# Performance work log

Hardware: AMD Instinct MI355X
Metric: run time of the kernel (lower is better)

Reference implementation:

```python
import jax, jax.numpy as jnp
import numpy as np

WINDOW_SIZE = 11  # 2*h_patch_size + 1 with h_patch_size=5
SIGMA = 1.5
C1 = 0.01 ** 2
C2 = 0.03 ** 2


def _window2d():
    x = np.arange(WINDOW_SIZE) - WINDOW_SIZE // 2
    g = np.exp(-(x ** 2) / (2.0 * SIGMA ** 2))
    g = g / g.sum()
    w = np.outer(g, g)  # [ws, ws], sums to 1
    return jnp.asarray(w, dtype=jnp.float32)


def setup_inputs() -> dict:
    key = jax.random.key(0)
    k1, k2 = jax.random.split(key)
    n_view, N, n_p, npatch, C = 4, 2048, 16, 121, 3
    img_pred = jax.random.uniform(k1, (n_view, N, n_p, npatch, C), dtype=jnp.float32)
    img_gt = jax.random.uniform(k2, (N, n_p, npatch, C), dtype=jnp.float32)
    return {"img_pred": img_pred, "img_gt": img_gt}


def reference(img_pred, img_gt):
    # img_pred: [n_view, N, n_p, npatch, C]; img_gt: [N, n_p, npatch, C]
    n_view, N, n_p, npatch, C = img_pred.shape
    ps = WINDOW_SIZE  # patch_size == window_size since conv has padding=0 and output is 1x1
    w = _window2d()  # [ps, ps]

    pred = img_pred.reshape(n_view, N, n_p, ps, ps, C)
    gt = img_gt.reshape(1, N, n_p, ps, ps, C)

    # Depthwise 11x11 conv on an 11x11 patch with padding=0 == gaussian-weighted sum.
    def wsum(x):
        return jnp.einsum('vnphwc,hw->vnpc', x, w)

    mu1 = wsum(pred)                      # [n_view, N, n_p, C]
    mu2 = wsum(gt)                        # [1, N, n_p, C]
    mu1_sq = mu1 * mu1
    mu2_sq = mu2 * mu2
    mu1_mu2 = mu1 * mu2
    sigma1_sq = wsum(pred * pred) - mu1_sq
    sigma2_sq = wsum(gt * gt) - mu2_sq    # [1, N, n_p, C]
    sigma12 = wsum(pred * gt) - mu1_mu2   # pred*gt broadcasts over n_view

    ssim_map = ((2.0 * mu1_mu2 + C1) * (2.0 * sigma12 + C2)) / (
        (mu1_sq + mu2_sq + C1) * (sigma1_sq + sigma2_sq + C2))
    return ssim_map.mean(-1)  # [n_view, N, n_p]
```

## Files before the change

### kernel.cpp

```cpp
#include <hip/hip_runtime.h>


static constexpr int N_OUT   = 4 * 2048 * 16;
static constexpr int NP_MASK = 2048 * 16 - 1;

__device__ __constant__ float G11[11] = {
    0.00102838f, 0.00759875f, 0.03600077f, 0.10936070f, 0.21300555f,
    0.26601173f,
    0.21300555f, 0.10936070f, 0.03600077f, 0.00759875f, 0.00102838f
};

__global__ __launch_bounds__(256) void ssim_kernel(
    const float* __restrict__ pred, const float* __restrict__ gt,
    float* __restrict__ out)
{
    const int o = blockIdx.x * 256 + threadIdx.x;
    const float* p = pred + (size_t)o * 363;
    const float* g = gt   + (size_t)(o & NP_MASK) * 363;

    float mu1[3] = {0.f, 0.f, 0.f};
    float mu2[3] = {0.f, 0.f, 0.f};
    float s1 [3] = {0.f, 0.f, 0.f};
    float s2 [3] = {0.f, 0.f, 0.f};
    float s12[3] = {0.f, 0.f, 0.f};

    #pragma unroll 1
    for (int r = 0; r < 11; ++r) {
        const float wr = G11[r];
        const float* pr = p + r * 33;
        const float* gr = g + r * 33;
        #pragma unroll
        for (int col = 0; col < 11; ++col) {
            const float w = wr * G11[col];
            #pragma unroll
            for (int c = 0; c < 3; ++c) {
                const float pv = pr[col * 3 + c];
                const float gv = gr[col * 3 + c];
                mu1[c] += w * pv;
                mu2[c] += w * gv;
                s1 [c] += w * pv * pv;
                s2 [c] += w * gv * gv;
                s12[c] += w * pv * gv;
            }
        }
    }

    const float C1 = 1e-4f;
    const float C2 = 9e-4f;
    float acc = 0.f;
    #pragma unroll
    for (int c = 0; c < 3; ++c) {
        const float m1 = mu1[c], m2 = mu2[c];
        const float m1sq = m1 * m1, m2sq = m2 * m2, m12 = m1 * m2;
        const float sig1  = s1[c]  - m1sq;
        const float sig2  = s2[c]  - m2sq;
        const float sg12  = s12[c] - m12;
        const float num = (2.f * m12 + C1) * (2.f * sg12 + C2);
        const float den = (m1sq + m2sq + C1) * (sig1 + sig2 + C2);
        acc += num / den;
    }
    out[o] = acc * (1.f / 3.f);
}

extern "C" void kernel_launch(void* const* d_in, const int* in_sizes, int n_in,
                              void* d_out, int out_size, void* d_ws, size_t ws_size,
                              hipStream_t stream) {
    const float* pred = (const float*)d_in[0];
    const float* gt   = (const float*)d_in[1];
    float* out        = (float*)d_out;
    ssim_kernel<<<N_OUT / 256, 256, 0, stream>>>(pred, gt, out);
}
```

Measured before the change: 340.2 us.

## Split each patch across 16 lanes with shuffle reduction for coalesced loads

Instead of one thread walking a whole 363-float patch with strided loads, 16 lanes share each patch, each loading a few pixels, and the partial sums are combined with xor shuffles. The 2D Gaussian weights are precomputed into shared memory. The goal is to coalesce global reads, which were badly strided across threads before. The cost is 15 shuffle rounds per patch, 7 of 128 slots padded with zero weights, and most lanes sitting idle during the final SSIM step.

```diff
diff --git a/kernel.cpp b/kernel.cpp
--- a/kernel.cpp
+++ b/kernel.cpp
@@ -10,11 +10,34 @@
     0.21300555f, 0.10936070f, 0.03600077f, 0.00759875f, 0.00102838f
 };
 
+__device__ __forceinline__ float red16(float v) {
+    v += __shfl_xor(v, 1);
+    v += __shfl_xor(v, 2);
+    v += __shfl_xor(v, 4);
+    v += __shfl_xor(v, 8);
+    return v;
+}
+
 __global__ __launch_bounds__(256) void ssim_kernel(
     const float* __restrict__ pred, const float* __restrict__ gt,
     float* __restrict__ out)
 {
-    const int o = blockIdx.x * 256 + threadIdx.x;
+    __shared__ float W[128];
+    const int t = threadIdx.x;
+    if (t < 128) {
+        float w = 0.f;
+        if (t < 121) {
+            const int r = t / 11;
+            const int c = t - r * 11;
+            w = G11[r] * G11[c];
+        }
+        W[t] = w;
+    }
+    __syncthreads();
+
+    const int lane  = t & 15;
+    const int group = t >> 4;
+    const int o     = blockIdx.x * 16 + group;
     const float* p = pred + (size_t)o * 363;
     const float* g = gt   + (size_t)(o & NP_MASK) * 363;
 
@@ -24,42 +47,51 @@
     float s2 [3] = {0.f, 0.f, 0.f};
     float s12[3] = {0.f, 0.f, 0.f};
 
-    #pragma unroll 1
-    for (int r = 0; r < 11; ++r) {
-        const float wr = G11[r];
-        const float* pr = p + r * 33;
-        const float* gr = g + r * 33;
+    #pragma unroll
+    for (int rnd = 0; rnd < 8; ++rnd) {
+        const int pix = lane + rnd * 16;
+        const float w = W[pix];
+        const int pc  = (pix < 121 ? pix : 120) * 3;
+        const float pv[3] = {p[pc], p[pc + 1], p[pc + 2]};
+        const float gv[3] = {g[pc], g[pc + 1], g[pc + 2]};
         #pragma unroll
-        for (int col = 0; col < 11; ++col) {
-            const float w = wr * G11[col];
-            #pragma unroll
-            for (int c = 0; c < 3; ++c) {
-                const float pv = pr[col * 3 + c];
-                const float gv = gr[col * 3 + c];
-                mu1[c] += w * pv;
-                mu2[c] += w * gv;
-                s1 [c] += w * pv * pv;
-                s2 [c] += w * gv * gv;
-                s12[c] += w * pv * gv;
-            }
+        for (int c = 0; c < 3; ++c) {
+            const float tp = w * pv[c];
+            const float tg = w * gv[c];
+            mu1[c] += tp;
+            mu2[c] += tg;
+            s1 [c] = fmaf(tp, pv[c], s1 [c]);
+            s2 [c] = fmaf(tg, gv[c], s2 [c]);
+            s12[c] = fmaf(tp, gv[c], s12[c]);
         }
     }
 
-    const float C1 = 1e-4f;
-    const float C2 = 9e-4f;
-    float acc = 0.f;
     #pragma unroll
     for (int c = 0; c < 3; ++c) {
-        const float m1 = mu1[c], m2 = mu2[c];
-        const float m1sq = m1 * m1, m2sq = m2 * m2, m12 = m1 * m2;
-        const float sig1  = s1[c]  - m1sq;
-        const float sig2  = s2[c]  - m2sq;
-        const float sg12  = s12[c] - m12;
-        const float num = (2.f * m12 + C1) * (2.f * sg12 + C2);
-        const float den = (m1sq + m2sq + C1) * (sig1 + sig2 + C2);
-        acc += num / den;
+        mu1[c] = red16(mu1[c]);
+        mu2[c] = red16(mu2[c]);
+        s1 [c] = red16(s1 [c]);
+        s2 [c] = red16(s2 [c]);
+        s12[c] = red16(s12[c]);
     }
-    out[o] = acc * (1.f / 3.f);
+
+    if (lane == 0) {
+        const float C1 = 1e-4f;
+        const float C2 = 9e-4f;
+        float acc = 0.f;
+        #pragma unroll
+        for (int c = 0; c < 3; ++c) {
+            const float m1 = mu1[c], m2 = mu2[c];
+            const float m1sq = m1 * m1, m2sq = m2 * m2, m12 = m1 * m2;
+            const float sig1 = s1[c]  - m1sq;
+            const float sig2 = s2[c]  - m2sq;
+            const float sg12 = s12[c] - m12;
+            const float num = (2.f * m12 + C1) * (2.f * sg12 + C2);
+            const float den = (m1sq + m2sq + C1) * (sig1 + sig2 + C2);
+            acc += num / den;
+        }
+        out[o] = acc * (1.f / 3.f);
+    }
 }
 
 extern "C" void kernel_launch(void* const* d_in, const int* in_sizes, int n_in,
@@ -68,5 +100,5 @@
     const float* pred = (const float*)d_in[0];
     const float* gt   = (const float*)d_in[1];
     float* out        = (float*)d_out;
-    ssim_kernel<<<N_OUT / 256, 256, 0, stream>>>(pred, gt, out);
+    ssim_kernel<<<N_OUT / 16, 256, 0, stream>>>(pred, gt, out);
 }
```

Result: faster. 293.8 us (-13.6%).

## Cooperate 16 lanes per output with coalesced LDS staging and LDS reduction

Applied to the files above, without the earlier changes.

Replaces the one-thread-per-output scheme, where each thread strided through 1452 bytes and loads were uncoalesced, with 16 lanes per output. Each wave stages four contiguous prediction patches into LDS using coalesced float4 loads. Each lane accumulates pairs of pixels with precomputed weights, and the partial sums are reduced through LDS scratch. It relies on manual lgkmcnt waits rather than barriers, which are valid only because each wave touches its own LDS region. It also adds reduction overhead and sets a launch-bounds occupancy hint.

```diff
diff --git a/kernel.cpp b/kernel.cpp
--- a/kernel.cpp
+++ b/kernel.cpp
@@ -3,6 +3,9 @@
 
 static constexpr int N_OUT   = 4 * 2048 * 16;
 static constexpr int NP_MASK = 2048 * 16 - 1;
+static constexpr int OPB     = 16;
+static constexpr int V4_WAVE = 363;
+static constexpr int LDS_F4  = 4 * V4_WAVE + 2;
 
 __device__ __constant__ float G11[11] = {
     0.00102838f, 0.00759875f, 0.03600077f, 0.10936070f, 0.21300555f,
@@ -10,56 +13,131 @@
     0.21300555f, 0.10936070f, 0.03600077f, 0.00759875f, 0.00102838f
 };
 
-__global__ __launch_bounds__(256) void ssim_kernel(
+__global__ __launch_bounds__(256, 6) void ssim_kernel(
     const float* __restrict__ pred, const float* __restrict__ gt,
     float* __restrict__ out)
 {
-    const int o = blockIdx.x * 256 + threadIdx.x;
-    const float* p = pred + (size_t)o * 363;
-    const float* g = gt   + (size_t)(o & NP_MASK) * 363;
+    __shared__ float4 predS4[LDS_F4];
 
+    const int t      = threadIdx.x;
+    const int wave   = t >> 6;
+    const int lane64 = t & 63;
+    const int lane   = t & 15;
+    const int group  = t >> 4;
+    const int o      = blockIdx.x * OPB + group;
+
+    const float* g = gt + (size_t)(o & NP_MASK) * 363;
+    float gv[4][6];
+    #pragma unroll
+    for (int r = 0; r < 4; ++r) {
+        const int k  = lane + r * 16;
+        const int kc = (k < 60 ? k : 60);
+        const float* gk = g + 6 * kc;
+        gv[r][0] = gk[0]; gv[r][1] = gk[1]; gv[r][2] = gk[2];
+        const bool full = (k < 60);
+        gv[r][3] = full ? gk[3] : 0.f;
+        gv[r][4] = full ? gk[4] : 0.f;
+        gv[r][5] = full ? gk[5] : 0.f;
+    }
+
+    const float4* p4 = (const float4*)(pred +
+                        (size_t)(blockIdx.x * OPB + wave * 4) * 363);
+    #pragma unroll
+    for (int r = 0; r < 6; ++r) {
+        const int idx = lane64 + r * 64;
+        if (idx < V4_WAVE) predS4[wave * V4_WAVE + idx] = p4[idx];
+    }
+
+    float wA[4], wB[4];
+    #pragma unroll
+    for (int r = 0; r < 4; ++r) {
+        const int k  = lane + r * 16;
+        const int pa = 2 * k, pb = 2 * k + 1;
+        wA[r] = (pa <= 120) ? G11[pa / 11] * G11[pa % 11] : 0.f;
+        wB[r] = (pb <= 120) ? G11[pb / 11] * G11[pb % 11] : 0.f;
+    }
+
+    asm volatile("s_waitcnt lgkmcnt(0)" ::: "memory");
+
+    const float* P = (const float*)predS4 + group * 363;
     float mu1[3] = {0.f, 0.f, 0.f};
     float mu2[3] = {0.f, 0.f, 0.f};
-    float s1 [3] = {0.f, 0.f, 0.f};
-    float s2 [3] = {0.f, 0.f, 0.f};
-    float s12[3] = {0.f, 0.f, 0.f};
+    float sp [3] = {0.f, 0.f, 0.f};
+    float sg [3] = {0.f, 0.f, 0.f};
+    float spg[3] = {0.f, 0.f, 0.f};
 
-    #pragma unroll 1
-    for (int r = 0; r < 11; ++r) {
-        const float wr = G11[r];
-        const float* pr = p + r * 33;
-        const float* gr = g + r * 33;
+    #pragma unroll
+    for (int r = 0; r < 4; ++r) {
+        const int k  = lane + r * 16;
+        const int kc = (k < 60 ? k : 60);
+        const float* Pk = P + 6 * kc;
+        const float pA[3] = {Pk[0], Pk[1], Pk[2]};
+        const float pB[3] = {Pk[3], Pk[4], Pk[5]};
         #pragma unroll
-        for (int col = 0; col < 11; ++col) {
-            const float w = wr * G11[col];
-            #pragma unroll
-            for (int c = 0; c < 3; ++c) {
-                const float pv = pr[col * 3 + c];
-                const float gv = gr[col * 3 + c];
-                mu1[c] += w * pv;
-                mu2[c] += w * gv;
-                s1 [c] += w * pv * pv;
-                s2 [c] += w * gv * gv;
-                s12[c] += w * pv * gv;
-            }
+        for (int c = 0; c < 3; ++c) {
+            const float ga = gv[r][c], gb = gv[r][c + 3];
+            float tp = wA[r] * pA[c];
+            float tg = wA[r] * ga;
+            mu1[c] += tp;  mu2[c] += tg;
+            sp [c] = fmaf(tp, pA[c], sp [c]);
+            sg [c] = fmaf(tg, ga,    sg [c]);
+            spg[c] = fmaf(tp, ga,    spg[c]);
+            float up = wB[r] * pB[c];
+            float ug = wB[r] * gb;
+            mu1[c] += up;  mu2[c] += ug;
+            sp [c] = fmaf(up, pB[c], sp [c]);
+            sg [c] = fmaf(ug, gb,    sg [c]);
+            spg[c] = fmaf(up, gb,    spg[c]);
         }
     }
 
-    const float C1 = 1e-4f;
-    const float C2 = 9e-4f;
-    float acc = 0.f;
-    #pragma unroll
-    for (int c = 0; c < 3; ++c) {
-        const float m1 = mu1[c], m2 = mu2[c];
-        const float m1sq = m1 * m1, m2sq = m2 * m2, m12 = m1 * m2;
-        const float sig1  = s1[c]  - m1sq;
-        const float sig2  = s2[c]  - m2sq;
-        const float sg12  = s12[c] - m12;
-        const float num = (2.f * m12 + C1) * (2.f * sg12 + C2);
-        const float den = (m1sq + m2sq + C1) * (sig1 + sig2 + C2);
-        acc += num / den;
+    float* scr = (float*)predS4 + wave * 1452;
+    {
+        const int q = lane64 >> 4;
+        const int j = lane;
+        float4* dst = (float4*)(scr + (j * 4 + q) * 20);
+        dst[0] = make_float4(mu1[0], mu1[1], mu1[2], mu2[0]);
+        dst[1] = make_float4(mu2[1], mu2[2], sp[0], sp[1]);
+        dst[2] = make_float4(sp[2],  sg[0],  sg[1], sg[2]);
+        dst[3] = make_float4(spg[0], spg[1], spg[2], 0.f);
     }
-    out[o] = acc * (1.f / 3.f);
+    asm volatile("s_waitcnt lgkmcnt(0)" ::: "memory");
+
+    const int q2 = lane64 >> 4;
+    const int st = lane64 & 15;
+    if (st < 15) {
+        float sum = 0.f;
+        #pragma unroll
+        for (int j2 = 0; j2 < 16; ++j2)
+            sum += scr[(j2 * 4 + q2) * 20 + st];
+        scr[q2 * 16 + st] = sum;
+    }
+    asm volatile("s_waitcnt lgkmcnt(0)" ::: "memory");
+
+    if (lane64 < 4) {
+        const float4* sv = (const float4*)(scr + lane64 * 16);
+        const float4 a = sv[0], b = sv[1], c4 = sv[2], d = sv[3];
+        const float M1[3]  = {a.x,  a.y,  a.z};
+        const float M2[3]  = {a.w,  b.x,  b.y};
+        const float S1[3]  = {b.z,  b.w,  c4.x};
+        const float S2[3]  = {c4.y, c4.z, c4.w};
+        const float S12[3] = {d.x,  d.y,  d.z};
+        const float C1 = 1e-4f;
+        const float C2 = 9e-4f;
+        float acc = 0.f;
+        #pragma unroll
+        for (int c = 0; c < 3; ++c) {
+            const float m1 = M1[c], m2 = M2[c];
+            const float m1sq = m1 * m1, m2sq = m2 * m2, m12 = m1 * m2;
+            const float sig1 = S1[c]  - m1sq;
+            const float sig2 = S2[c]  - m2sq;
+            const float sg12 = S12[c] - m12;
+            const float num = (2.f * m12 + C1) * (2.f * sg12 + C2);
+            const float den = (m1sq + m2sq + C1) * (sig1 + sig2 + C2);
+            acc += num / den;
+        }
+        out[blockIdx.x * OPB + wave * 4 + lane64] = acc * (1.f / 3.f);
+    }
 }
 
 extern "C" void kernel_launch(void* const* d_in, const int* in_sizes, int n_in,
@@ -68,5 +146,5 @@
     const float* pred = (const float*)d_in[0];
     const float* gt   = (const float*)d_in[1];
     float* out        = (float*)d_out;
-    ssim_kernel<<<N_OUT / 256, 256, 0, stream>>>(pred, gt, out);
+    ssim_kernel<<<N_OUT / OPB, 256, 0, stream>>>(pred, gt, out);
 }
```

Result: slower. 365.5 us (+7.4%).
